# Performance work log

Hardware: AMD Instinct MI355X
Metric: run time of the kernel (lower is better)

Reference implementation:

```python
import jax, jax.numpy as jnp
import numpy as np

N, K, H = 98, 10, 4        # landmarks, neighbors/node, heads
B, CIN, HC = 1024, 256, 64 # batch, in_channels, head_channels
NEG = -9e15


def setup_inputs() -> dict:
    key = jax.random.key(0)
    ks = jax.random.split(key, 3)
    rng = np.random.default_rng(0)
    # fixed sparsity pattern: K unique neighbors per row, row-major order
    cols2d = np.stack([np.sort(rng.choice(N, K, replace=False)) for _ in range(N)])
    rows = np.repeat(np.arange(N), K)
    cols = cols2d.reshape(-1)
    x = jax.random.normal(ks[0], (B, N, CIN), jnp.float32)
    W = jax.random.normal(ks[1], (H, 2, CIN, HC), jnp.float32) * 0.05  # xavier-ish
    e = jnp.ones((H, N * K), jnp.float32)  # nn.init.constant_(e, 1)
    stdv = 1.0 / np.sqrt(HC)
    bias = jax.random.uniform(ks[2], (H, HC), jnp.float32, -stdv, stdv)
    return {"x": x, "W": W, "e": e, "bias": bias,
            "rows": jnp.asarray(rows, jnp.int32),
            "cols": jnp.asarray(cols, jnp.int32)}


def reference(x, W, e, bias, rows, cols):
    # h0/h1 for all heads at once: [2, H, B, N, HC]
    h = jnp.einsum('bnc,hscd->shbnd', x, W)
    h0, h1 = h[0], h[1]
    # masked adjacency logits per head: -9e15 everywhere, learned e at edges
    base = jnp.full((N, N), NEG, jnp.float32)
    logits = jax.vmap(lambda eh: base.at[rows, cols].set(eh))(e)  # [H,N,N]
    A = jax.nn.softmax(logits, axis=-1)  # F.softmax(adj, dim=1) on [N,N]
    diag = jnp.diagonal(A, axis1=-2, axis2=-1)  # [H,N] -> adj*M part
    A_off = A - diag[..., None] * jnp.eye(N, dtype=A.dtype)  # adj*(1-M)
    out = diag[:, None, :, None] * h0 + jnp.einsum('hij,hbjd->hbid', A_off, h1)
    out = out + bias[:, None, None, :]  # [H,B,N,HC]
    # concat heads along channel dim -> [B, N, H*HC]
    return jnp.transpose(out, (1, 2, 0, 3)).reshape(B, N, H * HC)
```

## Files before the change

kernel.cpp:

```cpp
#include <hip/hip_runtime.h>

typedef __bf16 bf16;
typedef bf16 bf16x4 __attribute__((ext_vector_type(4)));
typedef bf16 bf16x8 __attribute__((ext_vector_type(8)));
typedef _Float16 half_t;
typedef half_t half4 __attribute__((ext_vector_type(4)));
typedef half_t half8 __attribute__((ext_vector_type(8)));
typedef float f32x4 __attribute__((ext_vector_type(4)));

#define NND 98
#define KNB 10
#define NH 4
#define CIN 256
#define HC 64
#define KAG 224
#define SROW 232
#define XA_TILE (7 * 8 * 64 * 8)

#define WP_OFF   0
#define WP_BYTES 262144
#define G2A_OFF  (WP_OFF + WP_BYTES)
#define G2A_BYTES (NH * 49 * 64 * 8 * 2)
#define XA_OFF   (G2A_OFF + G2A_BYTES)

__device__ __forceinline__ bf16x8 load_a8(const float* p) {
  f32x4 u = *(const f32x4*)p;
  f32x4 v = *(const f32x4*)(p + 4);
  bf16x8 a;
  a[0] = (bf16)u[0]; a[1] = (bf16)u[1]; a[2] = (bf16)u[2]; a[3] = (bf16)u[3];
  a[4] = (bf16)v[0]; a[5] = (bf16)v[1]; a[6] = (bf16)v[2]; a[7] = (bf16)v[3];
  return a;
}

__global__ __launch_bounds__(256) void prep_kernel(const float* __restrict__ W,
                                                   bf16* __restrict__ Wp,
                                                   const float* __restrict__ e,
                                                   const int* __restrict__ cols,
                                                   half_t* __restrict__ G2a,
                                                   const float* __restrict__ x,
                                                   bf16* __restrict__ xa, int B) {
  if (blockIdx.x < 64) {
    int t = blockIdx.x * 256 + threadIdx.x;
    int lane = t & 63;
    int nt = (t >> 6) & 3;
    int kt = (t >> 8) & 7;
    int hs = t >> 11;
    int n = nt * 16 + (lane & 15);
    int kb = kt * 32 + (lane >> 4) * 8;
    const float* src = W + (hs * CIN + kb) * HC + n;
    bf16x8 v;
#pragma unroll
    for (int j = 0; j < 8; ++j) v[j] = (bf16)src[j * HC];
    *(bf16x8*)(Wp + (long long)t * 8) = v;
    return;
  }
  if (blockIdx.x < 68) {
    __shared__ __align__(16) half_t g[112 * KAG];
    const int h = blockIdx.x - 64;
    const int tid = threadIdx.x;
    for (int i = tid; i < 112 * KAG / 2; i += 256) ((unsigned int*)g)[i] = 0u;
    __syncthreads();
    if (tid < NND) {
      const int i = tid;
      const int* cp = cols + i * KNB;
      const float* ep = e + (h * NND + i) * KNB;
      float ev[KNB];
      int cv[KNB];
      float mx = -3.0e38f;
#pragma unroll
      for (int j = 0; j < KNB; ++j) { cv[j] = cp[j]; ev[j] = ep[j]; mx = fmaxf(mx, ev[j]); }
      float s = 0.f;
#pragma unroll
      for (int j = 0; j < KNB; ++j) { ev[j] = __expf(ev[j] - mx); s += ev[j]; }
      const float inv = 1.f / s;
      float dg = 0.f;
#pragma unroll
      for (int j = 0; j < KNB; ++j) {
        float wj = ev[j] * inv;
        if (cv[j] == i) { dg = wj; wj = 0.f; }
        g[i * KAG + cv[j]] = (half_t)wj;
      }
      g[i * KAG + 112 + i] = (half_t)dg;
    }
    __syncthreads();
    for (int u = tid; u < 49 * 64; u += 256) {
      const int lane = u & 63;
      const int q = u >> 6;
      const int kt = q % 7;
      const int mt = q / 7;
      const int row = mt * 16 + (lane & 15);
      const int k0 = kt * 32 + (lane >> 4) * 8;
      half8 v = *(const half8*)(g + row * KAG + k0);
      *(half8*)(G2a + (((long long)h * 49 + q) * 64 + lane) * 8) = v;
    }
    return;
  }
  const int Bq = (B + 3) >> 2;
  int u = (blockIdx.x - 68) * 256 + threadIdx.x;
  if (u >= Bq * 7 * 8 * 64) return;
  const int lane = u & 63;
  const int kt = (u >> 6) & 7;
  const int v = u >> 9;
  const int b0 = v / 7;
  const int mt = v - b0 * 7;
  const int row = mt * 16 + (lane & 15);
  const int k0 = kt * 32 + (lane >> 4) * 8;
  bf16x8 a[4];
#pragma unroll
  for (int q = 0; q < 4; ++q) {
    const int b = b0 + Bq * q;
    a[q] = bf16x8{};
    if (b < B && row < NND) a[q] = load_a8(x + ((long long)b * NND + row) * CIN + k0);
  }
#pragma unroll
  for (int q = 0; q < 4; ++q) {
    const int b = b0 + Bq * q;
    if (b < B)
      *(bf16x8*)(xa + ((((long long)b * 7 + mt) * 8 + kt) * 64 + lane) * 8) = a[q];
  }
}

__global__ __launch_bounds__(512, 4) void semgconv_kernel(
    const bf16* __restrict__ xa, const half_t* __restrict__ G2a,
    const bf16* __restrict__ Wp, const float* __restrict__ bias,
    float* __restrict__ out, int nwg) {
  __shared__ __align__(16) unsigned char smem[65536];
  bf16* Wl = (bf16*)smem;
  half_t* S = (half_t*)smem;

  const int tid = threadIdx.x;
  const int lane = tid & 63;
  const int wv = tid >> 6;

  int n = blockIdx.x;
  int w = ((nwg & 7) == 0) ? ((n & 7) * (nwg >> 3) + (n >> 3)) : n;
  const int bp = w >> 2;
  const int h = w & 3;
  const int b0 = bp * 2;

  const int wm = wv & 3;
  const int sh = wv >> 2;
  const int mt0 = wm * 2;
  const bool has1 = (mt0 + 1 < 7);

  const bf16* ax0 = xa + (((long long)b0 * 7 + mt0) * 8 * 64 + lane) * 8;
  const bf16* ax1 = ax0 + XA_TILE;
  bf16x8 a00 = *(const bf16x8*)(ax0);
  bf16x8 a10 = *(const bf16x8*)(ax1);
  bf16x8 a01 = {}, a11 = {};
  if (has1) {
    a01 = *(const bf16x8*)(ax0 + 4096);
    a11 = *(const bf16x8*)(ax1 + 4096);
  }

  {
    const f32x4* src = (const f32x4*)(Wp + (long long)h * 32768);
    f32x4* dst = (f32x4*)smem;
#pragma unroll
    for (int it = 0; it < 8; ++it) {
      const int idx = tid + it * 512;
      dst[idx] = src[idx];
    }
  }
  __syncthreads();

  f32x4 acc[2][2][4] = {};
  {
    const bf16* wll = Wl + sh * 16384 + lane * 8;
#pragma unroll
    for (int kt = 0; kt < 8; ++kt) {
      bf16x8 n00, n10, n01, n11;
      if (kt < 7) {
        n00 = *(const bf16x8*)(ax0 + (kt + 1) * 512);
        n10 = *(const bf16x8*)(ax1 + (kt + 1) * 512);
        if (has1) {
          n01 = *(const bf16x8*)(ax0 + 4096 + (kt + 1) * 512);
          n11 = *(const bf16x8*)(ax1 + 4096 + (kt + 1) * 512);
        }
      }
      bf16x8 bfr[4];
#pragma unroll
      for (int nt = 0; nt < 4; ++nt)
        bfr[nt] = *(const bf16x8*)(wll + (kt * 4 + nt) * 512);
#pragma unroll
      for (int nt = 0; nt < 4; ++nt) {
        acc[0][0][nt] = __builtin_amdgcn_mfma_f32_16x16x32_bf16(a00, bfr[nt], acc[0][0][nt], 0, 0, 0);
        acc[1][0][nt] = __builtin_amdgcn_mfma_f32_16x16x32_bf16(a10, bfr[nt], acc[1][0][nt], 0, 0, 0);
      }
      if (has1) {
#pragma unroll
        for (int nt = 0; nt < 4; ++nt) {
          acc[0][1][nt] = __builtin_amdgcn_mfma_f32_16x16x32_bf16(a01, bfr[nt], acc[0][1][nt], 0, 0, 0);
          acc[1][1][nt] = __builtin_amdgcn_mfma_f32_16x16x32_bf16(a11, bfr[nt], acc[1][1][nt], 0, 0, 0);
        }
      }
      a00 = n00; a10 = n10; a01 = n01; a11 = n11;
    }
  }
  __syncthreads();

  {
    const int jb = (sh ? 0 : 112) + (lane >> 4) * 4;
    const int cb = lane & 15;
#pragma unroll
    for (int it2 = 0; it2 < 2; ++it2) {
#pragma unroll
      for (int im = 0; im < 2; ++im) {
        if (mt0 + im < 7) {
          const int j0 = jb + (mt0 + im) * 16;
#pragma unroll
          for (int nt = 0; nt < 4; ++nt) {
            half4 hv;
            hv[0] = (half_t)acc[it2][im][nt][0];
            hv[1] = (half_t)acc[it2][im][nt][1];
            hv[2] = (half_t)acc[it2][im][nt][2];
            hv[3] = (half_t)acc[it2][im][nt][3];
            *(half4*)(&S[it2 * (64 * SROW) + (nt * 16 + cb) * SROW + j0]) = hv;
          }
        }
      }
    }
  }
  __syncthreads();

  const int it2 = wv & 1;
  const int wm2 = wv >> 1;
  const int mt0b = wm2 * 2;
  const bool has1b = (mt0b + 1 < 7);
  f32x4 a2[2][4] = {};
  {
    const half_t* g2l = G2a + ((long long)(h * 49 + mt0b * 7) * 64 + lane) * 8;
    const half_t* sl = S + it2 * (64 * SROW) + (lane & 15) * SROW + (lane >> 4) * 8;
    half8 af0 = *(const half8*)(g2l);
    half8 af1 = {};
    if (has1b) af1 = *(const half8*)(g2l + 7 * 512);
#pragma unroll
    for (int kt = 0; kt < 7; ++kt) {
      half8 n0, n1;
      if (kt < 6) {
        n0 = *(const half8*)(g2l + (long long)(kt + 1) * 512);
        if (has1b) n1 = *(const half8*)(g2l + (long long)(8 + kt) * 512);
      }
      half8 bfr[4];
#pragma unroll
      for (int nt = 0; nt < 4; ++nt)
        bfr[nt] = *(const half8*)(sl + nt * 16 * SROW + kt * 32);
#pragma unroll
      for (int nt = 0; nt < 4; ++nt) {
        a2[0][nt] = __builtin_amdgcn_mfma_f32_16x16x32_f16(af0, bfr[nt], a2[0][nt], 0, 0, 0);
        if (has1b)
          a2[1][nt] = __builtin_amdgcn_mfma_f32_16x16x32_f16(af1, bfr[nt], a2[1][nt], 0, 0, 0);
      }
      af0 = n0; af1 = n1;
    }
  }

  {
    const int cb = lane & 15;
    const int r0 = (lane >> 4) * 4;
    float bs[4];
#pragma unroll
    for (int nt = 0; nt < 4; ++nt) bs[nt] = bias[h * HC + nt * 16 + cb];
    float* ob = out + (long long)(b0 + it2) * NND * (NH * HC) + h * HC + cb;
#pragma unroll
    for (int im = 0; im < 2; ++im) {
      const int mt = mt0b + im;
      if (mt < 7) {
#pragma unroll
        for (int r = 0; r < 4; ++r) {
          const int row = mt * 16 + r0 + r;
          if (row < NND) {
#pragma unroll
            for (int nt = 0; nt < 4; ++nt)
              ob[(long long)row * (NH * HC) + nt * 16] = a2[im][nt][r] + bs[nt];
          }
        }
      }
    }
  }
}

extern "C" void kernel_launch(void* const* d_in, const int* in_sizes, int n_in,
                              void* d_out, int out_size, void* d_ws, size_t ws_size,
                              hipStream_t stream) {
  const float* x    = (const float*)d_in[0];
  const float* W    = (const float*)d_in[1];
  const float* e    = (const float*)d_in[2];
  const float* bias = (const float*)d_in[3];
  const int* cols   = (const int*)d_in[5];
  float* out        = (float*)d_out;

  int B = in_sizes[0] / (NND * CIN);

  bf16* Wp    = (bf16*)((char*)d_ws + WP_OFF);
  half_t* G2a = (half_t*)((char*)d_ws + G2A_OFF);
  bf16* xa    = (bf16*)((char*)d_ws + XA_OFF);

  const int Bq = (B + 3) >> 2;
  const int xa_blocks = (Bq * 7 * 8 * 64 + 255) / 256;
  prep_kernel<<<68 + xa_blocks, 256, 0, stream>>>(W, Wp, e, cols, G2a, x, xa, B);

  const int nwg = (B / 2) * NH;
  semgconv_kernel<<<nwg, 512, 0, stream>>>(xa, G2a, Wp, bias, out, nwg);
}
```

Before: 230.5 us.

## Apply diagonal term elementwise instead of folding it into the aggregation GEMM

The diagonal self-weight part (diag * h0) was previously handled by concatenating h0 into the K dimension of the second MFMA GEMM (K=224, 7 k-tiles). It is now computed elementwise: the prep kernel writes per-node diagonal weights, the h0 accumulators are scaled by them and staged in a separate LDS buffer, and they are added in the epilogue. This shrinks the aggregation GEMM to K=128 (4 k-tiles) and the G2a matrix accordingly. The cost is an extra LDS region, extra zero-padding writes and an fp16 rounding of the scaled diagonal term.

```diff
diff --git a/kernel.cpp b/kernel.cpp
--- a/kernel.cpp
+++ b/kernel.cpp
@@ -13,15 +13,20 @@
 #define NH 4
 #define CIN 256
 #define HC 64
-#define KAG 224
-#define SROW 232
+#define SKP 136
+#define D0R 120
+#define S_HALFS (64 * SKP)
+#define S_BYTES (2 * S_HALFS * 2)
+#define D0_HALFS (64 * D0R)
 #define XA_TILE (7 * 8 * 64 * 8)
 
 #define WP_OFF   0
 #define WP_BYTES 262144
 #define G2A_OFF  (WP_OFF + WP_BYTES)
-#define G2A_BYTES (NH * 49 * 64 * 8 * 2)
-#define XA_OFF   (G2A_OFF + G2A_BYTES)
+#define G2A_BYTES (NH * 28 * 64 * 8 * 2)
+#define DIAG_OFF (G2A_OFF + G2A_BYTES)
+#define DIAG_BYTES 2048
+#define XA_OFF   (DIAG_OFF + DIAG_BYTES)
 
 __device__ __forceinline__ bf16x8 load_a8(const float* p) {
   f32x4 u = *(const f32x4*)p;
@@ -37,6 +42,7 @@
                                                    const float* __restrict__ e,
                                                    const int* __restrict__ cols,
                                                    half_t* __restrict__ G2a,
+                                                   float* __restrict__ diagb,
                                                    const float* __restrict__ x,
                                                    bf16* __restrict__ xa, int B) {
   if (blockIdx.x < 64) {
@@ -55,10 +61,10 @@
     return;
   }
   if (blockIdx.x < 68) {
-    __shared__ __align__(16) half_t g[112 * KAG];
+    __shared__ __align__(16) half_t g[112 * 128];
     const int h = blockIdx.x - 64;
     const int tid = threadIdx.x;
-    for (int i = tid; i < 112 * KAG / 2; i += 256) ((unsigned int*)g)[i] = 0u;
+    for (int i = tid; i < 112 * 128 / 2; i += 256) ((unsigned int*)g)[i] = 0u;
     __syncthreads();
     if (tid < NND) {
       const int i = tid;
@@ -78,20 +84,22 @@
       for (int j = 0; j < KNB; ++j) {
         float wj = ev[j] * inv;
         if (cv[j] == i) { dg = wj; wj = 0.f; }
-        g[i * KAG + cv[j]] = (half_t)wj;
-      }
-      g[i * KAG + 112 + i] = (half_t)dg;
+        g[i * 128 + cv[j]] = (half_t)wj;
+      }
+      diagb[h * 112 + i] = dg;
+    } else if (tid < 112) {
+      diagb[h * 112 + tid] = 0.f;
     }
     __syncthreads();
-    for (int u = tid; u < 49 * 64; u += 256) {
+    for (int u = tid; u < 28 * 64; u += 256) {
       const int lane = u & 63;
       const int q = u >> 6;
-      const int kt = q % 7;
-      const int mt = q / 7;
+      const int kt = q & 3;
+      const int mt = q >> 2;
       const int row = mt * 16 + (lane & 15);
       const int k0 = kt * 32 + (lane >> 4) * 8;
-      half8 v = *(const half8*)(g + row * KAG + k0);
-      *(half8*)(G2a + (((long long)h * 49 + q) * 64 + lane) * 8) = v;
+      half8 v = *(const half8*)(g + row * 128 + k0);
+      *(half8*)(G2a + (((long long)h * 28 + q) * 64 + lane) * 8) = v;
     }
     return;
   }
@@ -122,11 +130,12 @@
 
 __global__ __launch_bounds__(512, 4) void semgconv_kernel(
     const bf16* __restrict__ xa, const half_t* __restrict__ G2a,
-    const bf16* __restrict__ Wp, const float* __restrict__ bias,
-    float* __restrict__ out, int nwg) {
+    const bf16* __restrict__ Wp, const float* __restrict__ diagb,
+    const float* __restrict__ bias, float* __restrict__ out, int nwg) {
   __shared__ __align__(16) unsigned char smem[65536];
   bf16* Wl = (bf16*)smem;
   half_t* S = (half_t*)smem;
+  half_t* D0 = (half_t*)(smem + S_BYTES);
 
   const int tid = threadIdx.x;
   const int lane = tid & 63;
@@ -142,6 +151,12 @@
   const int sh = wv >> 2;
   const int mt0 = wm * 2;
   const bool has1 = (mt0 + 1 < 7);
+  const int cb = lane & 15;
+  const int rsub = (lane >> 4) * 4;
+
+  f32x4 dg[2];
+  dg[0] = *(const f32x4*)(diagb + h * 112 + mt0 * 16 + rsub);
+  dg[1] = has1 ? *(const f32x4*)(diagb + h * 112 + (mt0 + 1) * 16 + rsub) : f32x4{};
 
   const bf16* ax0 = xa + (((long long)b0 * 7 + mt0) * 8 * 64 + lane) * 8;
   const bf16* ax1 = ax0 + XA_TILE;
@@ -199,15 +214,13 @@
   }
   __syncthreads();
 
-  {
-    const int jb = (sh ? 0 : 112) + (lane >> 4) * 4;
-    const int cb = lane & 15;
+  if (sh) {
 #pragma unroll
     for (int it2 = 0; it2 < 2; ++it2) {
 #pragma unroll
       for (int im = 0; im < 2; ++im) {
         if (mt0 + im < 7) {
-          const int j0 = jb + (mt0 + im) * 16;
+          const int j0 = (mt0 + im) * 16 + rsub;
 #pragma unroll
           for (int nt = 0; nt < 4; ++nt) {
             half4 hv;
@@ -215,11 +228,36 @@
             hv[1] = (half_t)acc[it2][im][nt][1];
             hv[2] = (half_t)acc[it2][im][nt][2];
             hv[3] = (half_t)acc[it2][im][nt][3];
-            *(half4*)(&S[it2 * (64 * SROW) + (nt * 16 + cb) * SROW + j0]) = hv;
+            *(half4*)(&S[it2 * S_HALFS + (nt * 16 + cb) * SKP + j0]) = hv;
           }
         }
       }
     }
+  } else {
+#pragma unroll
+    for (int it2 = 0; it2 < 2; ++it2) {
+#pragma unroll
+      for (int im = 0; im < 2; ++im) {
+        if (mt0 + im < 7) {
+          const int j0 = (mt0 + im) * 16 + rsub;
+#pragma unroll
+          for (int nt = 0; nt < 4; ++nt) {
+            half4 hv;
+            hv[0] = (half_t)(dg[im][0] * acc[it2][im][nt][0]);
+            hv[1] = (half_t)(dg[im][1] * acc[it2][im][nt][1]);
+            hv[2] = (half_t)(dg[im][2] * acc[it2][im][nt][2]);
+            hv[3] = (half_t)(dg[im][3] * acc[it2][im][nt][3]);
+            *(half4*)(&D0[it2 * D0_HALFS + (nt * 16 + cb) * D0R + j0]) = hv;
+          }
+        }
+      }
+    }
+  }
+  if (tid < 256) {
+    const int it = tid >> 7;
+    const int c = (tid >> 1) & 63;
+    const int sg = tid & 1;
+    *(half8*)(&S[it * S_HALFS + c * SKP + 112 + sg * 8]) = half8{};
   }
   __syncthreads();
 
@@ -229,22 +267,22 @@
   const bool has1b = (mt0b + 1 < 7);
   f32x4 a2[2][4] = {};
   {
-    const half_t* g2l = G2a + ((long long)(h * 49 + mt0b * 7) * 64 + lane) * 8;
-    const half_t* sl = S + it2 * (64 * SROW) + (lane & 15) * SROW + (lane >> 4) * 8;
+    const half_t* g2l = G2a + ((long long)(h * 28 + mt0b * 4) * 64 + lane) * 8;
+    const half_t* sl = S + it2 * S_HALFS + cb * SKP + (lane >> 4) * 8;
     half8 af0 = *(const half8*)(g2l);
     half8 af1 = {};
-    if (has1b) af1 = *(const half8*)(g2l + 7 * 512);
-#pragma unroll
-    for (int kt = 0; kt < 7; ++kt) {
-      half8 n0, n1;
-      if (kt < 6) {
-        n0 = *(const half8*)(g2l + (long long)(kt + 1) * 512);
-        if (has1b) n1 = *(const half8*)(g2l + (long long)(8 + kt) * 512);
+    if (has1b) af1 = *(const half8*)(g2l + 4 * 512);
+#pragma unroll
+    for (int kt = 0; kt < 4; ++kt) {
+      half8 n0 = {}, n1 = {};
+      if (kt < 3) {
+        n0 = *(const half8*)(g2l + (kt + 1) * 512);
+        if (has1b) n1 = *(const half8*)(g2l + (4 + kt + 1) * 512);
       }
       half8 bfr[4];
 #pragma unroll
       for (int nt = 0; nt < 4; ++nt)
-        bfr[nt] = *(const half8*)(sl + nt * 16 * SROW + kt * 32);
+        bfr[nt] = *(const half8*)(sl + nt * 16 * SKP + kt * 32);
 #pragma unroll
       for (int nt = 0; nt < 4; ++nt) {
         a2[0][nt] = __builtin_amdgcn_mfma_f32_16x16x32_f16(af0, bfr[nt], a2[0][nt], 0, 0, 0);
@@ -256,8 +294,6 @@
   }
 
   {
-    const int cb = lane & 15;
-    const int r0 = (lane >> 4) * 4;
     float bs[4];
 #pragma unroll
     for (int nt = 0; nt < 4; ++nt) bs[nt] = bias[h * HC + nt * 16 + cb];
@@ -267,12 +303,13 @@
       const int mt = mt0b + im;
       if (mt < 7) {
 #pragma unroll
-        for (int r = 0; r < 4; ++r) {
-          const int row = mt * 16 + r0 + r;
-          if (row < NND) {
-#pragma unroll
-            for (int nt = 0; nt < 4; ++nt)
-              ob[(long long)row * (NH * HC) + nt * 16] = a2[im][nt][r] + bs[nt];
+        for (int nt = 0; nt < 4; ++nt) {
+          half4 dv = *(const half4*)(&D0[it2 * D0_HALFS + (nt * 16 + cb) * D0R + mt * 16 + rsub]);
+#pragma unroll
+          for (int r = 0; r < 4; ++r) {
+            const int row = mt * 16 + rsub + r;
+            if (row < NND)
+              ob[(long long)row * (NH * HC) + nt * 16] = a2[im][nt][r] + (float)dv[r] + bs[nt];
           }
         }
       }
@@ -292,14 +329,15 @@
 
   int B = in_sizes[0] / (NND * CIN);
 
-  bf16* Wp    = (bf16*)((char*)d_ws + WP_OFF);
-  half_t* G2a = (half_t*)((char*)d_ws + G2A_OFF);
-  bf16* xa    = (bf16*)((char*)d_ws + XA_OFF);
+  bf16* Wp     = (bf16*)((char*)d_ws + WP_OFF);
+  half_t* G2a  = (half_t*)((char*)d_ws + G2A_OFF);
+  float* diagb = (float*)((char*)d_ws + DIAG_OFF);
+  bf16* xa     = (bf16*)((char*)d_ws + XA_OFF);
 
   const int Bq = (B + 3) >> 2;
   const int xa_blocks = (Bq * 7 * 8 * 64 + 255) / 256;
-  prep_kernel<<<68 + xa_blocks, 256, 0, stream>>>(W, Wp, e, cols, G2a, x, xa, B);
+  prep_kernel<<<68 + xa_blocks, 256, 0, stream>>>(W, Wp, e, cols, G2a, diagb, x, xa, B);
 
   const int nwg = (B / 2) * NH;
-  semgconv_kernel<<<nwg, 512, 0, stream>>>(xa, G2a, Wp, bias, out, nwg);
+  semgconv_kernel<<<nwg, 512, 0, stream>>>(xa, G2a, Wp, diagb, bias, out, nwg);
 }
```

Result: slower. 252.3 us (+9.5%).
